# Performance work log

Measured on AMD Instinct MI355X. Metric: run time of the kernel, lower is better.

## Reference

```python
import jax, jax.numpy as jnp
import numpy as np

ALPHA = 0.5  # leakage
T, B, I, H = 512, 64, 128, 1024
SCALE = 0.9  # input_scaling
RHO = 0.99   # target spectral radius (approximated by 1/sqrt(H) normal scaling)


def setup_inputs() -> dict:
    key = jax.random.key(0)
    k1, k2, k3, k4, k5 = jax.random.split(key, 5)
    x = jax.random.normal(k1, (T, B, I), dtype=jnp.float32)
    # uniform(-scale, scale) kernel init
    W_in0 = jax.random.uniform(k2, (H, I), jnp.float32, -SCALE, SCALE)
    # normal recurrent init scaled so spectral radius ~= rho (circular law: radius ~ sigma*sqrt(H))
    W_hat0 = jax.random.normal(k3, (H, H), jnp.float32) * (RHO / np.sqrt(H))
    W_in1 = jax.random.uniform(k4, (H, H), jnp.float32, -SCALE, SCALE)
    W_hat1 = jax.random.normal(k5, (H, H), jnp.float32) * (RHO / np.sqrt(H))
    return {"x": x, "W_in0": W_in0, "W_hat0": W_hat0, "W_in1": W_in1, "W_hat1": W_hat1}


def _run_layer(inp, W_in, W_hat):
    # inp: [T, B, F_in]; returns full state trajectory [T, B, H]
    def step(h, x_t):
        pre = x_t @ W_in.T + h @ W_hat.T          # [B, H]
        h_new = (1.0 - ALPHA) * h + ALPHA * jnp.tanh(pre)
        return h_new, h_new

    h0 = jnp.zeros((inp.shape[1], W_hat.shape[0]), dtype=inp.dtype)
    _, ys = jax.lax.scan(step, h0, inp)
    return ys


def reference(x, W_in0, W_hat0, W_in1, W_hat1):
    e0 = _run_layer(x, W_in0, W_hat0)   # layer 0 states [T, B, H]
    e1 = _run_layer(e0, W_in1, W_hat1)  # layer 1 states [T, B, H]
    return jnp.stack([e0, e1], axis=-2)  # [T, B, num_layers, H]
```

## Files before the change

### kernel.cpp

```cpp
#include <hip/hip_runtime.h>
#include <math.h>

#define TSTEPS 512
#define BATCH  64
#define HDIM   1024
#define IDIM   128
#define NBLOCKS 256
#define NTHR   512

typedef __attribute__((ext_vector_type(8))) short bf16x8;
typedef __attribute__((ext_vector_type(4))) float f32x4;
typedef __attribute__((ext_vector_type(4))) unsigned u32x4;

#define WI0HI 0
#define WI0LO (WI0HI + 1024*128)
#define WH0HI (WI0LO + 1024*128)
#define WH0LO (WH0HI + 1024*1024)
#define WI1HI (WH0LO + 1024*1024)
#define WI1LO (WI1HI + 1024*1024)
#define WH1HI (WI1LO + 1024*1024)
#define WH1LO (WH1HI + 1024*1024)
#define WS_USHORTS (WH1LO + 1024*1024)
#define CNT_OFF_BYTES ((size_t)WS_USHORTS * 2)
#define BAR_BYTES (256 * 64)

__device__ __forceinline__ unsigned short bf_hi(float f) {
    unsigned u = __builtin_bit_cast(unsigned, f);
    unsigned r = u + 0x7fffu + ((u >> 16) & 1u);
    return (unsigned short)(r >> 16);
}
__device__ __forceinline__ float bf_tof(unsigned short h) {
    unsigned u = ((unsigned)h) << 16;
    return __builtin_bit_cast(float, u);
}

__device__ __forceinline__ void split8v(f32x4 a, f32x4 b,
                                        bf16x8& ah, bf16x8& al) {
    float fv[8] = {a[0], a[1], a[2], a[3], b[0], b[1], b[2], b[3]};
    u32x4 H, L;
    #pragma unroll
    for (int q = 0; q < 4; ++q) {
        const float f0 = fv[2 * q], f1 = fv[2 * q + 1];
        unsigned h;
        asm("v_cvt_pk_bf16_f32 %0, %1, %2" : "=v"(h) : "v"(f0), "v"(f1));
        const float h0 = __builtin_bit_cast(float, h << 16);
        const float h1 = __builtin_bit_cast(float, h & 0xffff0000u);
        unsigned lo;
        asm("v_cvt_pk_bf16_f32 %0, %1, %2" : "=v"(lo) : "v"(f0 - h0), "v"(f1 - h1));
        H[q] = h; L[q] = lo;
    }
    ah = __builtin_bit_cast(bf16x8, H);
    al = __builtin_bit_cast(bf16x8, L);
}

__device__ __forceinline__ void ks_r2(f32x4 a, f32x4 b,
                                      bf16x8 bh, bf16x8 bl, f32x4& acc) {
    bf16x8 ah, al;
    split8v(a, b, ah, al);
    acc = __builtin_amdgcn_mfma_f32_16x16x32_bf16(ah, bh, acc, 0, 0, 0);
    acc = __builtin_amdgcn_mfma_f32_16x16x32_bf16(al, bh, acc, 0, 0, 0);
    acc = __builtin_amdgcn_mfma_f32_16x16x32_bf16(ah, bl, acc, 0, 0, 0);
}

#define LD2(B, base, g) _Pragma("unroll") for (int c = 0; c < 2; ++c) { \
    (B)[2*c]   = *(const f32x4*)((base) + ((g)*2 + c) * 32); \
    (B)[2*c+1] = *(const f32x4*)((base) + ((g)*2 + c) * 32 + 4); }
#define PR2(B, wOff, g) _Pragma("unroll") for (int c = 0; c < 2; ++c) { \
    ks_r2((B)[2*c], (B)[2*c+1], wfh[(wOff)+(g)*2+c], wfl[(wOff)+(g)*2+c], \
          ((((g)*2+c) & 1) ? accA : accB)); }

__global__ void prep_kernel(const float* __restrict__ Wi0, const float* __restrict__ Wh0,
                            const float* __restrict__ Wi1, const float* __restrict__ Wh1,
                            unsigned short* __restrict__ wsU)
{
    const int n = 1024*128 + 3*1024*1024;
    for (int e = blockIdx.x * blockDim.x + threadIdx.x; e < n;
         e += gridDim.x * blockDim.x) {
        const float* src; int idx, hiOff, loOff;
        if (e < 1024*128)            { src = Wi0; idx = e;              hiOff = WI0HI; loOff = WI0LO; }
        else if (e < 1024*128 + 1024*1024)   { src = Wh0; idx = e - 1024*128;   hiOff = WH0HI; loOff = WH0LO; }
        else if (e < 1024*128 + 2*1024*1024) { src = Wi1; idx = e - 1024*128 - 1024*1024; hiOff = WI1HI; loOff = WI1LO; }
        else                         { src = Wh1; idx = e - 1024*128 - 2*1024*1024; hiOff = WH1HI; loOff = WH1LO; }
        float f = src[idx];
        unsigned short h = bf_hi(f);
        wsU[hiOff + idx] = h;
        wsU[loOff + idx] = bf_hi(f - bf_tof(h));
    }
}

__device__ __forceinline__ void wave_wait(unsigned* cnt, unsigned epoch,
                                          int baseLine, int mask) {
    const int lane = (int)(threadIdx.x & 63);
    unsigned* p = cnt + (unsigned)(baseLine + (lane & mask)) * 16;
    for (;;) {
        unsigned v = __hip_atomic_load(p, __ATOMIC_RELAXED, __HIP_MEMORY_SCOPE_AGENT);
        if (__ballot(v >= epoch) == ~0ull) break;
        __builtin_amdgcn_s_sleep(1);
    }
}

__global__ __launch_bounds__(NTHR, 2) void reservoir_kernel(
    const float* __restrict__ x, float* __restrict__ out,
    const unsigned short* __restrict__ wsU, unsigned* __restrict__ cnt)
{
    __shared__ f32x4 red[8 * 64];

    const int bid = blockIdx.x;
    const int layer = bid >> 7;
    const int rr  = bid & 127;
    const int jt  = rr >> 1, mh = rr & 1;
    const int dom = layer * 2 + mh;
    const int tid = (int)threadIdx.x;
    const int w   = __builtin_amdgcn_readfirstlane(tid >> 6);
    const int m2  = w & 1, kh = w >> 1;
    const int l   = tid & 63, lr = l & 15, tq = l >> 4;
    const int jbase = jt * 16;
    const int arow  = mh * 32 + m2 * 16 + lr;

    bf16x8 wfh[16], wfl[16];
    if (layer == 0) {
        const size_t rx = (size_t)(jbase + lr) * IDIM + kh * 32 + tq * 8;
        wfh[0] = *(const bf16x8*)(wsU + WI0HI + rx);
        wfl[0] = *(const bf16x8*)(wsU + WI0LO + rx);
        const size_t rh = (size_t)(jbase + lr) * HDIM + kh * 256 + tq * 8;
        #pragma unroll
        for (int ks = 0; ks < 8; ++ks) {
            wfh[1 + ks] = *(const bf16x8*)(wsU + WH0HI + rh + ks * 32);
            wfl[1 + ks] = *(const bf16x8*)(wsU + WH0LO + rh + ks * 32);
        }
    } else {
        const int hiOff = (kh < 2) ? WI1HI : WH1HI;
        const int loOff = (kh < 2) ? WI1LO : WH1LO;
        const size_t ro = (size_t)(jbase + lr) * HDIM + (kh & 1) * 512 + tq * 8;
        #pragma unroll
        for (int ks = 0; ks < 16; ++ks) {
            wfh[ks] = *(const bf16x8*)(wsU + hiOff + ro + ks * 32);
            wfl[ks] = *(const bf16x8*)(wsU + loOff + ro + ks * 32);
        }
    }

    const int rowLocal = tid >> 4;
    const int colF = tid & 15;
    const int m2f = rowLocal >> 4, tqf = (rowLocal >> 2) & 3, rf = rowLocal & 3;
    const int lf  = tqf * 16 + colF;
    float hold = 0.f;

    for (int i = 0; i <= TSTEPS; ++i) {
        const int t = layer ? (i - 1) : i;
        const bool valid = layer ? (t >= 0) : (t < TSTEPS);
        if (valid) {
            f32x4 accA = {0.f, 0.f, 0.f, 0.f};
            f32x4 accB = {0.f, 0.f, 0.f, 0.f};
            if (layer == 0) {
                {
                    const float* xs = x + (size_t)t * (BATCH * IDIM) + arow * IDIM + kh * 32 + tq * 8;
                    ks_r2(*(const f32x4*)xs, *(const f32x4*)(xs + 4), wfh[0], wfl[0], accA);
                }
                if (t >= 1) {
                    wave_wait(cnt, (unsigned)i, mh * 64 + kh * 16, 15);
                    const float* h0 = out + (size_t)(t - 1) * 131072 + arow * 2048
                                      + kh * 256 + tq * 8;
                    f32x4 bA[4], bB[4];
                    LD2(bA, h0, 0); LD2(bB, h0, 1);
                    PR2(bA, 1, 0); LD2(bA, h0, 2);
                    PR2(bB, 1, 1); LD2(bB, h0, 3);
                    PR2(bA, 1, 2); PR2(bB, 1, 3);
                }
            } else {
                if ((kh < 2) || (t >= 1)) {
                    const int ts  = (kh < 2) ? t : (t - 1);
                    const int pbase = (kh < 2) ? (mh * 64 + kh * 32)
                                               : ((2 + mh) * 64 + (kh - 2) * 32);
                    wave_wait(cnt, (unsigned)i, pbase, 31);
                    const float* src = out + (size_t)ts * 131072 + arow * 2048
                                       + ((kh < 2) ? 0 : 1024) + (kh & 1) * 512 + tq * 8;
                    f32x4 bA[4], bB[4];
                    LD2(bA, src, 0); LD2(bB, src, 1);
                    PR2(bA, 0, 0); LD2(bA, src, 2);
                    PR2(bB, 0, 1); LD2(bB, src, 3);
                    PR2(bA, 0, 2); LD2(bA, src, 4);
                    PR2(bB, 0, 3); LD2(bB, src, 5);
                    PR2(bA, 0, 4); LD2(bA, src, 6);
                    PR2(bB, 0, 5); LD2(bB, src, 7);
                    PR2(bA, 0, 6); PR2(bB, 0, 7);
                }
            }

            red[w * 64 + l] = accA + accB;
            __syncthreads();
            {
                float s = 0.f;
                #pragma unroll
                for (int k4 = 0; k4 < 4; ++k4)
                    s += red[(k4 * 2 + m2f) * 64 + lf][rf];
                const float hnew = 0.5f * hold + 0.5f * tanhf(s);
                hold = hnew;
                const int row = mh * 32 + rowLocal;
                float* dst = out + (size_t)t * 131072 + row * 2048 + layer * 1024 + jbase + colF;
                __hip_atomic_store(dst, hnew, __ATOMIC_RELAXED, __HIP_MEMORY_SCOPE_AGENT);
            }
        }
        if (i < TSTEPS) {
            __syncthreads();
            if (tid == 0)
                __hip_atomic_store(cnt + (unsigned)(dom * 64 + jt) * 16,
                                   (unsigned)(i + 1),
                                   __ATOMIC_RELAXED, __HIP_MEMORY_SCOPE_AGENT);
        }
    }
}

extern "C" void kernel_launch(void* const* d_in, const int* in_sizes, int n_in,
                              void* d_out, int out_size, void* d_ws, size_t ws_size,
                              hipStream_t stream) {
    const float* x   = (const float*)d_in[0];
    const float* Wi0 = (const float*)d_in[1];
    const float* Wh0 = (const float*)d_in[2];
    const float* Wi1 = (const float*)d_in[3];
    const float* Wh1 = (const float*)d_in[4];
    float* out = (float*)d_out;
    unsigned short* wsU = (unsigned short*)d_ws;
    unsigned* cnt = (unsigned*)((char*)d_ws + CNT_OFF_BYTES);

    hipMemsetAsync((char*)d_ws + CNT_OFF_BYTES, 0, BAR_BYTES, stream);
    prep_kernel<<<256, 256, 0, stream>>>(Wi0, Wh0, Wi1, Wh1, wsU);

    void* args[] = {(void*)&x, (void*)&out, (void*)&wsU, (void*)&cnt};
    hipLaunchCooperativeKernel((const void*)reservoir_kernel,
                               dim3(NBLOCKS), dim3(NTHR), args, 0, stream);
}
```

Baseline: 4.208 ms.

## Use per-wave completion flags and double-buffered reduction to drop block barrier

Each wave now publishes its own completion flag after its stores drain, and consumers wait only on the specific wave flags covering the rows they read, so the second per-step __syncthreads and the block-level flag go away. The reduction buffer is double-buffered by step parity so the next step's writes cannot overwrite data still being read without that barrier. The input-projection MFMA for layer 0 is moved after the hidden-state loads are issued, to overlap them. The cost is eight times more flag lines and more polling loads per wait, and correctness now depends on the mapping between waves and the rows they write.

New measurement: 4.652 ms. +10.5%, slower.

```diff
diff --git a/kernel.cpp b/kernel.cpp
--- a/kernel.cpp
+++ b/kernel.cpp
@@ -22,7 +22,7 @@
 #define WH1LO (WH1HI + 1024*1024)
 #define WS_USHORTS (WH1LO + 1024*1024)
 #define CNT_OFF_BYTES ((size_t)WS_USHORTS * 2)
-#define BAR_BYTES (256 * 64)
+#define BAR_BYTES (2048 * 64)
 
 __device__ __forceinline__ unsigned short bf_hi(float f) {
     unsigned u = __builtin_bit_cast(unsigned, f);
@@ -88,13 +88,22 @@
     }
 }
 
-__device__ __forceinline__ void wave_wait(unsigned* cnt, unsigned epoch,
-                                          int baseLine, int mask) {
-    const int lane = (int)(threadIdx.x & 63);
-    unsigned* p = cnt + (unsigned)(baseLine + (lane & mask)) * 16;
+__device__ __forceinline__ unsigned flag_ld(unsigned* cnt, int line) {
+    return __hip_atomic_load(cnt + (unsigned)line * 16, __ATOMIC_RELAXED,
+                             __HIP_MEMORY_SCOPE_AGENT);
+}
+
+__device__ __forceinline__ void wave_wait1(unsigned* cnt, unsigned epoch, int line) {
     for (;;) {
-        unsigned v = __hip_atomic_load(p, __ATOMIC_RELAXED, __HIP_MEMORY_SCOPE_AGENT);
-        if (__ballot(v >= epoch) == ~0ull) break;
+        if (__ballot(flag_ld(cnt, line) >= epoch) == ~0ull) break;
+        __builtin_amdgcn_s_sleep(1);
+    }
+}
+__device__ __forceinline__ void wave_wait2(unsigned* cnt, unsigned epoch,
+                                           int line1, int line2) {
+    for (;;) {
+        bool ok = (flag_ld(cnt, line1) >= epoch) & (flag_ld(cnt, line2) >= epoch);
+        if (__ballot(ok) == ~0ull) break;
         __builtin_amdgcn_s_sleep(1);
     }
 }
@@ -103,7 +112,7 @@
     const float* __restrict__ x, float* __restrict__ out,
     const unsigned short* __restrict__ wsU, unsigned* __restrict__ cnt)
 {
-    __shared__ f32x4 red[8 * 64];
+    __shared__ f32x4 red[2][8 * 64];
 
     const int bid = blockIdx.x;
     const int layer = bid >> 7;
@@ -116,6 +125,7 @@
     const int l   = tid & 63, lr = l & 15, tq = l >> 4;
     const int jbase = jt * 16;
     const int arow  = mh * 32 + m2 * 16 + lr;
+    const int myFlagLine = ((dom * 64 + jt) << 3) + w;
 
     bf16x8 wfh[16], wfl[16];
     if (layer == 0) {
@@ -145,6 +155,12 @@
     const int lf  = tqf * 16 + colF;
     float hold = 0.f;
 
+    const int l0_line = (((mh) * 64 + kh * 16 + (l >> 2)) << 3) + m2 * 4 + (l & 3);
+    const int pdom  = (kh < 2) ? mh : (2 + mh);
+    const int pbase = (kh < 2) ? (kh * 32) : ((kh - 2) * 32);
+    const int l1_line1 = ((pdom * 64 + pbase + (l >> 2)) << 3) + m2 * 4 + (l & 3);
+    const int l1_line2 = ((pdom * 64 + pbase + 16 + (l >> 2)) << 3) + m2 * 4 + (l & 3);
+
     for (int i = 0; i <= TSTEPS; ++i) {
         const int t = layer ? (i - 1) : i;
         const bool valid = layer ? (t >= 0) : (t < TSTEPS);
@@ -152,26 +168,26 @@
             f32x4 accA = {0.f, 0.f, 0.f, 0.f};
             f32x4 accB = {0.f, 0.f, 0.f, 0.f};
             if (layer == 0) {
-                {
-                    const float* xs = x + (size_t)t * (BATCH * IDIM) + arow * IDIM + kh * 32 + tq * 8;
-                    ks_r2(*(const f32x4*)xs, *(const f32x4*)(xs + 4), wfh[0], wfl[0], accA);
-                }
+                const float* xs = x + (size_t)t * (BATCH * IDIM) + arow * IDIM + kh * 32 + tq * 8;
+                const f32x4 xa = *(const f32x4*)xs;
+                const f32x4 xb = *(const f32x4*)(xs + 4);
                 if (t >= 1) {
-                    wave_wait(cnt, (unsigned)i, mh * 64 + kh * 16, 15);
+                    wave_wait1(cnt, (unsigned)i, l0_line);
                     const float* h0 = out + (size_t)(t - 1) * 131072 + arow * 2048
                                       + kh * 256 + tq * 8;
                     f32x4 bA[4], bB[4];
                     LD2(bA, h0, 0); LD2(bB, h0, 1);
+                    ks_r2(xa, xb, wfh[0], wfl[0], accA);
                     PR2(bA, 1, 0); LD2(bA, h0, 2);
                     PR2(bB, 1, 1); LD2(bB, h0, 3);
                     PR2(bA, 1, 2); PR2(bB, 1, 3);
+                } else {
+                    ks_r2(xa, xb, wfh[0], wfl[0], accA);
                 }
             } else {
                 if ((kh < 2) || (t >= 1)) {
                     const int ts  = (kh < 2) ? t : (t - 1);
-                    const int pbase = (kh < 2) ? (mh * 64 + kh * 32)
-                                               : ((2 + mh) * 64 + (kh - 2) * 32);
-                    wave_wait(cnt, (unsigned)i, pbase, 31);
+                    wave_wait2(cnt, (unsigned)i, l1_line1, l1_line2);
                     const float* src = out + (size_t)ts * 131072 + arow * 2048
                                        + ((kh < 2) ? 0 : 1024) + (kh & 1) * 512 + tq * 8;
                     f32x4 bA[4], bB[4];
@@ -186,24 +202,29 @@
                 }
             }
 
-            red[w * 64 + l] = accA + accB;
+            red[i & 1][w * 64 + l] = accA + accB;
             __syncthreads();
             {
                 float s = 0.f;
                 #pragma unroll
                 for (int k4 = 0; k4 < 4; ++k4)
-                    s += red[(k4 * 2 + m2f) * 64 + lf][rf];
+                    s += red[i & 1][(k4 * 2 + m2f) * 64 + lf][rf];
                 const float hnew = 0.5f * hold + 0.5f * tanhf(s);
                 hold = hnew;
                 const int row = mh * 32 + rowLocal;
                 float* dst = out + (size_t)t * 131072 + row * 2048 + layer * 1024 + jbase + colF;
                 __hip_atomic_store(dst, hnew, __ATOMIC_RELAXED, __HIP_MEMORY_SCOPE_AGENT);
             }
-        }
-        if (i < TSTEPS) {
-            __syncthreads();
-            if (tid == 0)
-                __hip_atomic_store(cnt + (unsigned)(dom * 64 + jt) * 16,
+            if (i < TSTEPS) {
+                asm volatile("s_waitcnt vmcnt(0)" ::: "memory");
+                if (l == 0)
+                    __hip_atomic_store(cnt + (unsigned)myFlagLine * 16,
+                                       (unsigned)(i + 1),
+                                       __ATOMIC_RELAXED, __HIP_MEMORY_SCOPE_AGENT);
+            }
+        } else if (i < TSTEPS) {
+            if (l == 0)
+                __hip_atomic_store(cnt + (unsigned)myFlagLine * 16,
                                    (unsigned)(i + 1),
                                    __ATOMIC_RELAXED, __HIP_MEMORY_SCOPE_AGENT);
         }
```
